# Kernel optimization log

Hardware: AMD Instinct MI355X
Metric: run time of the kernel (lower is better)

The kernel has to match this reference:

```python
import jax, jax.numpy as jnp
import numpy as np

B, T, K = 64, 1024, 128
START, STOP = K - 2, K - 1  # tag_dictionary['<START>'], tag_dictionary['<STOP>']
NEG = -10000.0


def setup_inputs() -> dict:
    key = jax.random.key(0)
    k1, k2, k3, k4 = jax.random.split(key, 4)
    feats = jax.random.normal(k1, (B, T, K), jnp.float32)
    tags = jax.random.randint(k2, (B, T), 0, K - 2)          # real labels only
    lens = jax.random.randint(k3, (B,), 1, T + 1)            # 1 <= len <= T
    transitions = jax.random.normal(k4, (K, K), jnp.float32)
    transitions = transitions.at[START, :].set(NEG).at[:, STOP].set(NEG)
    return {"feats": feats, "tags": tags, "lens": lens, "transitions": transitions}


def _forward_alg(feats, transitions, lens):
    # feats: [B, T, K]; CRF forward (log-partition) via scan over time.
    B_, T_, K_ = feats.shape
    # init: only START position kept from feats[:, 0, :], rest -10000
    alpha0 = jnp.full((B_, K_), NEG, feats.dtype).at[:, START].set(feats[:, 0, START])

    def step(alpha, feat_i):
        # tag_var[b, s, p] = feat_i[b, s] + transitions[s, p] + alpha[b, p]
        new = feat_i + jax.scipy.special.logsumexp(alpha[:, None, :] + transitions[None, :, :], axis=2)
        return new, new

    _, alphas = jax.lax.scan(step, alpha0, jnp.swapaxes(feats[:, 1:, :], 0, 1))  # [T-1, B, K]
    all_alphas = jnp.concatenate([alpha0[None], alphas], axis=0)  # [T, B, K]; idx t-1 == forward_var[:, t]
    terminal = all_alphas[lens - 1, jnp.arange(B_)]               # [B, K]
    return jax.scipy.special.logsumexp(terminal, axis=1)          # [B]


def _score_sentence(feats, transitions, tags, lens):
    B_, T_, K_ = feats.shape
    pos = jnp.arange(T_ - 1)
    # pad_stop_tags = tags[:, 1:] with positions >= len-1 replaced by STOP
    stop_tags = jnp.where(pos[None, :] >= (lens - 1)[:, None], STOP, tags[:, 1:])
    trans_sc = transitions[stop_tags, tags[:, :-1]]               # [B, T-1]
    tmask = (pos[None, :] < (lens - 1)[:, None]).astype(feats.dtype)
    emit = jnp.take_along_axis(feats, tags[:, :, None], axis=2)[:, :, 0]  # [B, T]
    emask = (jnp.arange(T_)[None, :] < lens[:, None]).astype(feats.dtype)
    return jnp.sum(trans_sc * tmask, axis=1) + jnp.sum(emit * emask, axis=1)


def reference(feats, tags, lens, transitions):
    forward_score = _forward_alg(feats, transitions, lens)
    gold_score = _score_sentence(feats, transitions, tags, lens)
    return jnp.mean(forward_score - gold_score)
```

## Files before the change

kernel.cpp:

```cpp
#include <hip/hip_runtime.h>
#include <math.h>

#define BB 64
#define TT 1024
#define KK 128
#define START_TAG 126
#define STOP_TAG 127
#define NTH 256
#define CS 64
#define EP 36

typedef float v2f __attribute__((ext_vector_type(2)));
typedef float v4f __attribute__((ext_vector_type(4)));

__device__ __forceinline__ void step_barrier() {
  asm volatile("s_waitcnt lgkmcnt(0)" ::: "memory");
  __builtin_amdgcn_s_barrier();
  asm volatile("" ::: "memory");
}

__device__ __forceinline__ float quad_add(float x) {
  int y = __builtin_amdgcn_update_dpp(0, __float_as_int(x), 0xB1, 0xF, 0xF, true);
  x = x + __int_as_float(y);
  y = __builtin_amdgcn_update_dpp(0, __float_as_int(x), 0x4E, 0xF, 0xF, true);
  return x + __int_as_float(y);
}
__device__ __forceinline__ float quad_max(float x) {
  int y = __builtin_amdgcn_update_dpp(0, __float_as_int(x), 0xB1, 0xF, 0xF, true);
  x = fmaxf(x, __int_as_float(y));
  y = __builtin_amdgcn_update_dpp(0, __float_as_int(x), 0x4E, 0xF, 0xF, true);
  return fmaxf(x, __int_as_float(y));
}

__global__ __launch_bounds__(NTH) void crf_forward(
    const float* __restrict__ feats,
    const int*   __restrict__ tags,
    const int*   __restrict__ lens,
    const float* __restrict__ trans,
    float*       __restrict__ out_pb)
{
  __shared__ __align__(16) float ebuf[2][4 * EP];
  __shared__ float sbuf[2];
  __shared__ __align__(16) float maxT_lds[KK];
  __shared__ __align__(16) float Fbuf[CS * KK];
  __shared__ float wsum[NTH / 64];

  const int tid = threadIdx.x;
  const int b   = blockIdx.x;
  const int q   = tid & 3;
  const int g   = tid >> 2;
  const int r0  = 2 * g;
  const int L   = lens[b];
  const float* fb = feats + (size_t)b * TT * KK;

  v2f Ea[16], Eb[16];
  float m0 = -INFINITY, m1 = -INFINITY;
  {
    const float* t0 = trans + (size_t)r0 * KK + q * 32;
    const float* t1 = t0 + KK;
    #pragma unroll
    for (int i = 0; i < 16; ++i) {
      Ea[i] = *(const v2f*)(t0 + 2 * i);
      Eb[i] = *(const v2f*)(t1 + 2 * i);
      m0 = fmaxf(m0, fmaxf(Ea[i][0], Ea[i][1]));
      m1 = fmaxf(m1, fmaxf(Eb[i][0], Eb[i][1]));
    }
  }
  m0 = quad_max(m0);
  m1 = quad_max(m1);
  #pragma unroll
  for (int i = 0; i < 16; ++i) {
    Ea[i][0] = __expf(Ea[i][0] - m0); Ea[i][1] = __expf(Ea[i][1] - m0);
    Eb[i][0] = __expf(Eb[i][0] - m1); Eb[i][1] = __expf(Eb[i][1] - m1);
  }
  if (q == 0) { maxT_lds[r0] = m0; maxT_lds[r0 + 1] = m1; }

  if (tid < KK)
    ebuf[0][(tid >> 5) * EP + (tid & 31)] = (tid == START_TAG) ? 1.0f : 0.0f;
  if (tid == 0) sbuf[0] = 1.0f;
  float M = fb[START_TAG];

  float4 pf[8];
  {
    const float4* s4 = (const float4*)fb;
    #pragma unroll
    for (int i = 0; i < 8; ++i) pf[i] = s4[i * NTH + tid];
  }

  step_barrier();

  const v4f mTv = *(const v4f*)(maxT_lds + (tid & 31) * 4);

  int p = 0;
  for (int c = 0; c * CS < L; ++c) {
    float4* Fb4 = (float4*)Fbuf;
    #pragma unroll
    for (int i = 0; i < 8; ++i) {
      float4 v = pf[i];
      float4 o;
      o.x = __expf(v.x + mTv[0]); o.y = __expf(v.y + mTv[1]);
      o.z = __expf(v.z + mTv[2]); o.w = __expf(v.w + mTv[3]);
      Fb4[i * NTH + tid] = o;
    }
    if ((c + 1) * CS < TT) {
      const float4* s4 = (const float4*)(fb + (size_t)(c + 1) * CS * KK);
      #pragma unroll
      for (int i = 0; i < 8; ++i) pf[i] = s4[i * NTH + tid];
    }
    step_barrier();

    const int t_end = (L < (c + 1) * CS) ? L : (c + 1) * CS;
    for (int t = (c == 0) ? 1 : c * CS; t < t_end; ++t) {
      const float* er = ebuf[p];
      float* ew = ebuf[p ^ 1];
      const float sp = sbuf[p];
      const v2f Fv = *(const v2f*)(Fbuf + (t & (CS - 1)) * KK + r0);
      float rr; asm("v_rcp_f32 %0, %1" : "=v"(rr) : "v"(sp));
      const float rF0 = rr * Fv[0];
      const float rF1 = rr * Fv[1];

      const v2f* e2 = (const v2f*)(er + q * EP);
      v2f a0 = {0.f,0.f}, a1 = {0.f,0.f}, a2 = {0.f,0.f}, a3 = {0.f,0.f};
      v2f b0 = {0.f,0.f}, b1 = {0.f,0.f}, b2 = {0.f,0.f}, b3 = {0.f,0.f};
      #pragma unroll
      for (int i = 0; i < 4; ++i) {
        v2f ea0 = e2[4 * i + 0], ea1 = e2[4 * i + 1];
        v2f ea2 = e2[4 * i + 2], ea3 = e2[4 * i + 3];
        a0 += ea0 * Ea[4 * i + 0];
        a1 += ea1 * Ea[4 * i + 1];
        a2 += ea2 * Ea[4 * i + 2];
        a3 += ea3 * Ea[4 * i + 3];
        b0 += ea0 * Eb[4 * i + 0];
        b1 += ea1 * Eb[4 * i + 1];
        b2 += ea2 * Eb[4 * i + 2];
        b3 += ea3 * Eb[4 * i + 3];
      }
      v2f as = (a0 + a1) + (a2 + a3);
      v2f bs = (b0 + b1) + (b2 + b3);
      float d0 = quad_add(as[0] + as[1]);
      float d1 = quad_add(bs[0] + bs[1]);

      v2f ev; ev[0] = d0 * rF0; ev[1] = d1 * rF1;
      if (q == 0)
        *(v2f*)(ew + (r0 >> 5) * EP + (r0 & 31)) = ev;
      if (tid == 252) sbuf[p ^ 1] = d0;
      if (tid < 64) M += __logf(sp);
      p ^= 1;
      step_barrier();
    }
  }

  float fwd = 0.f;
  {
    const float* efin = ebuf[p];
    if (tid < 64) {
      float sm = efin[(tid >> 5) * EP + (tid & 31)]
               + efin[((tid + 64) >> 5) * EP + ((tid + 64) & 31)];
      #pragma unroll
      for (int m = 1; m < 64; m <<= 1) sm += __shfl_xor(sm, m, 64);
      fwd = M + __logf(sm);
    }
  }

  float gg = 0.f;
  const int* tg = tags + b * TT;
  for (int t = tid; t < TT; t += NTH) {
    if (t < L)     gg += fb[(size_t)t * KK + tg[t]];
    if (t < L - 1) gg += trans[(size_t)tg[t + 1] * KK + tg[t]];
  }
  #pragma unroll
  for (int m = 1; m < 64; m <<= 1) gg += __shfl_xor(gg, m, 64);
  if ((tid & 63) == 0) wsum[tid >> 6] = gg;
  step_barrier();
  if (tid == 0) {
    float gold = 0.f;
    #pragma unroll
    for (int w = 0; w < NTH / 64; ++w) gold += wsum[w];
    out_pb[b] = fwd - gold;
  }
}

__global__ void crf_mean(const float* __restrict__ pb, float* __restrict__ out) {
  int tid = threadIdx.x;
  float v = pb[tid];
  #pragma unroll
  for (int m = 1; m < 64; m <<= 1) v += __shfl_xor(v, m, 64);
  if (tid == 0) out[0] = v * (1.0f / 64.0f);
}

extern "C" void kernel_launch(void* const* d_in, const int* in_sizes, int n_in,
                              void* d_out, int out_size, void* d_ws, size_t ws_size,
                              hipStream_t stream) {
  const float* feats = (const float*)d_in[0];
  const int*   tags  = (const int*)d_in[1];
  const int*   lens  = (const int*)d_in[2];
  const float* trans = (const float*)d_in[3];
  float* pb = (float*)d_ws;
  crf_forward<<<BB, NTH, 0, stream>>>(feats, tags, lens, trans, pb);
  crf_mean<<<1, 64, 0, stream>>>(pb, (float*)d_out);
}
```

Baseline: 435.4 us.

## Split each transition row across thread pairs with v4f dot products

Reworks the per-step matrix-vector work so each thread pair owns one output tag (each thread covers 64 columns) instead of quads owning two rows. The thread keeps 16 v4f registers of exp(transitions) and reads the alpha vector with 128-bit LDS loads. A single DPP pair add replaces the two-stage quad reduction, and the padded ebuf layout is dropped. Launch bounds now also state one block per CU. The aim is fewer LDS loads and shorter reduction latency on the serial time step, at the risk of LDS bank conflicts from the unpadded broadcast reads.

Measured after the change: 537.4 us. 23.4% more time.

```diff
diff --git a/kernel.cpp b/kernel.cpp
--- a/kernel.cpp
+++ b/kernel.cpp
@@ -8,9 +8,7 @@
 #define STOP_TAG 127
 #define NTH 256
 #define CS 64
-#define EP 36
 
-typedef float v2f __attribute__((ext_vector_type(2)));
 typedef float v4f __attribute__((ext_vector_type(4)));
 
 __device__ __forceinline__ void step_barrier() {
@@ -19,27 +17,23 @@
   asm volatile("" ::: "memory");
 }
 
-__device__ __forceinline__ float quad_add(float x) {
+__device__ __forceinline__ float pair_add(float x) {
   int y = __builtin_amdgcn_update_dpp(0, __float_as_int(x), 0xB1, 0xF, 0xF, true);
-  x = x + __int_as_float(y);
-  y = __builtin_amdgcn_update_dpp(0, __float_as_int(x), 0x4E, 0xF, 0xF, true);
   return x + __int_as_float(y);
 }
-__device__ __forceinline__ float quad_max(float x) {
+__device__ __forceinline__ float pair_max(float x) {
   int y = __builtin_amdgcn_update_dpp(0, __float_as_int(x), 0xB1, 0xF, 0xF, true);
-  x = fmaxf(x, __int_as_float(y));
-  y = __builtin_amdgcn_update_dpp(0, __float_as_int(x), 0x4E, 0xF, 0xF, true);
   return fmaxf(x, __int_as_float(y));
 }
 
-__global__ __launch_bounds__(NTH) void crf_forward(
+__global__ __launch_bounds__(NTH, 1) void crf_forward(
     const float* __restrict__ feats,
     const int*   __restrict__ tags,
     const int*   __restrict__ lens,
     const float* __restrict__ trans,
     float*       __restrict__ out_pb)
 {
-  __shared__ __align__(16) float ebuf[2][4 * EP];
+  __shared__ __align__(16) float ebuf[2][KK];
   __shared__ float sbuf[2];
   __shared__ __align__(16) float maxT_lds[KK];
   __shared__ __align__(16) float Fbuf[CS * KK];
@@ -47,36 +41,32 @@
 
   const int tid = threadIdx.x;
   const int b   = blockIdx.x;
-  const int q   = tid & 3;
-  const int g   = tid >> 2;
-  const int r0  = 2 * g;
+  const int r   = tid >> 1;
+  const int h   = tid & 1;
   const int L   = lens[b];
   const float* fb = feats + (size_t)b * TT * KK;
 
-  v2f Ea[16], Eb[16];
-  float m0 = -INFINITY, m1 = -INFINITY;
+#define EREGS(X) X(0) X(1) X(2) X(3) X(4) X(5) X(6) X(7) \
+                 X(8) X(9) X(10) X(11) X(12) X(13) X(14) X(15)
+#define DECLE(i) v4f E##i;
+  EREGS(DECLE)
+  float mT = -INFINITY;
   {
-    const float* t0 = trans + (size_t)r0 * KK + q * 32;
-    const float* t1 = t0 + KK;
-    #pragma unroll
-    for (int i = 0; i < 16; ++i) {
-      Ea[i] = *(const v2f*)(t0 + 2 * i);
-      Eb[i] = *(const v2f*)(t1 + 2 * i);
-      m0 = fmaxf(m0, fmaxf(Ea[i][0], Ea[i][1]));
-      m1 = fmaxf(m1, fmaxf(Eb[i][0], Eb[i][1]));
-    }
+    const v4f* tr = (const v4f*)(trans + (size_t)r * KK + h * 64);
+#define LOADE(i) E##i = tr[i];                                          \
+    mT = fmaxf(mT, fmaxf(fmaxf(E##i[0], E##i[1]), fmaxf(E##i[2], E##i[3])));
+    EREGS(LOADE)
   }
-  m0 = quad_max(m0);
-  m1 = quad_max(m1);
-  #pragma unroll
-  for (int i = 0; i < 16; ++i) {
-    Ea[i][0] = __expf(Ea[i][0] - m0); Ea[i][1] = __expf(Ea[i][1] - m0);
-    Eb[i][0] = __expf(Eb[i][0] - m1); Eb[i][1] = __expf(Eb[i][1] - m1);
-  }
-  if (q == 0) { maxT_lds[r0] = m0; maxT_lds[r0 + 1] = m1; }
+  mT = pair_max(mT);
+#define EXPE(i) {                                                       \
+    v4f v = E##i;                                                       \
+    v[0] = __expf(v[0] - mT); v[1] = __expf(v[1] - mT);                 \
+    v[2] = __expf(v[2] - mT); v[3] = __expf(v[3] - mT);                 \
+    E##i = v; }
+  EREGS(EXPE)
+  if (h == 0) maxT_lds[r] = mT;
 
-  if (tid < KK)
-    ebuf[0][(tid >> 5) * EP + (tid & 31)] = (tid == START_TAG) ? 1.0f : 0.0f;
+  if (tid < KK) ebuf[0][tid] = (tid == START_TAG) ? 1.0f : 0.0f;
   if (tid == 0) sbuf[0] = 1.0f;
   float M = fb[START_TAG];
 
@@ -111,40 +101,27 @@
 
     const int t_end = (L < (c + 1) * CS) ? L : (c + 1) * CS;
     for (int t = (c == 0) ? 1 : c * CS; t < t_end; ++t) {
-      const float* er = ebuf[p];
-      float* ew = ebuf[p ^ 1];
       const float sp = sbuf[p];
-      const v2f Fv = *(const v2f*)(Fbuf + (t & (CS - 1)) * KK + r0);
+      const float Fr = Fbuf[(t & (CS - 1)) * KK + r];
       float rr; asm("v_rcp_f32 %0, %1" : "=v"(rr) : "v"(sp));
-      const float rF0 = rr * Fv[0];
-      const float rF1 = rr * Fv[1];
+      const float rF = rr * Fr;
 
-      const v2f* e2 = (const v2f*)(er + q * EP);
-      v2f a0 = {0.f,0.f}, a1 = {0.f,0.f}, a2 = {0.f,0.f}, a3 = {0.f,0.f};
-      v2f b0 = {0.f,0.f}, b1 = {0.f,0.f}, b2 = {0.f,0.f}, b3 = {0.f,0.f};
-      #pragma unroll
-      for (int i = 0; i < 4; ++i) {
-        v2f ea0 = e2[4 * i + 0], ea1 = e2[4 * i + 1];
-        v2f ea2 = e2[4 * i + 2], ea3 = e2[4 * i + 3];
-        a0 += ea0 * Ea[4 * i + 0];
-        a1 += ea1 * Ea[4 * i + 1];
-        a2 += ea2 * Ea[4 * i + 2];
-        a3 += ea3 * Ea[4 * i + 3];
-        b0 += ea0 * Eb[4 * i + 0];
-        b1 += ea1 * Eb[4 * i + 1];
-        b2 += ea2 * Eb[4 * i + 2];
-        b3 += ea3 * Eb[4 * i + 3];
-      }
-      v2f as = (a0 + a1) + (a2 + a3);
-      v2f bs = (b0 + b1) + (b2 + b3);
-      float d0 = quad_add(as[0] + as[1]);
-      float d1 = quad_add(bs[0] + bs[1]);
+      const v4f* e4 = (const v4f*)(ebuf[p] + h * 64);
+      v4f a0 = {0.f,0.f,0.f,0.f}, a1 = a0, a2 = a0, a3 = a0;
+#define DOTE4(i0,i1,i2,i3)                                              \
+      a0 += e4[i0] * E##i0;                                             \
+      a1 += e4[i1] * E##i1;                                             \
+      a2 += e4[i2] * E##i2;                                             \
+      a3 += e4[i3] * E##i3;
+      DOTE4(0,1,2,3) DOTE4(4,5,6,7) DOTE4(8,9,10,11) DOTE4(12,13,14,15)
+      v4f av = (a0 + a1) + (a2 + a3);
+      const float half = (av[0] + av[1]) + (av[2] + av[3]);
+      const float d = pair_add(half);
 
-      v2f ev; ev[0] = d0 * rF0; ev[1] = d1 * rF1;
-      if (q == 0)
-        *(v2f*)(ew + (r0 >> 5) * EP + (r0 & 31)) = ev;
-      if (tid == 252) sbuf[p ^ 1] = d0;
-      if (tid < 64) M += __logf(sp);
+      const float ev = d * rF;
+      if (h == 0) ebuf[p ^ 1][r] = ev;
+      if (tid == 252) sbuf[p ^ 1] = d;
+      M += __logf(sp);
       p ^= 1;
       step_barrier();
     }
@@ -154,8 +131,7 @@
   {
     const float* efin = ebuf[p];
     if (tid < 64) {
-      float sm = efin[(tid >> 5) * EP + (tid & 31)]
-               + efin[((tid + 64) >> 5) * EP + ((tid + 64) & 31)];
+      float sm = efin[tid] + efin[tid + 64];
       #pragma unroll
       for (int m = 1; m < 64; m <<= 1) sm += __shfl_xor(sm, m, 64);
       fwd = M + __logf(sm);
```
